# Optimization experiments

Hardware: AMD Instinct MI355X
Metric: run time of the kernel (lower is better)

The kernel has to match this reference:

```python
import jax, jax.numpy as jnp
import numpy as np

# Dims from init_kwargs / input_specs
C_IN, H, W = 128, 224, 224
C_OUT, KH, KW = 256, 3, 3
STRIDE = 1  # padding='valid'


def setup_inputs() -> dict:
    key = jax.random.key(0)
    k1, k2 = jax.random.split(key)
    x = jax.random.normal(k1, (C_IN, H, W), dtype=jnp.float32)
    kernels = jax.random.normal(k2, (C_OUT, C_IN, KH, KW), dtype=jnp.float32) * 0.05
    return {"x": x, "kernels": kernels}


def reference(x, kernels):
    # Original does im2col + matmul, which is exactly a valid cross-correlation
    # (no kernel flip). Express it as a direct conv: (1,C,H,W) * (O,I,kh,kw).
    out = jax.lax.conv_general_dilated(
        x[None],                      # (1, C_in, H, W)
        kernels,                      # (C_out, C_in, KH, KW)
        window_strides=(STRIDE, STRIDE),
        padding="VALID",
        dimension_numbers=("NCHW", "OIHW", "NCHW"),
    )
    return out[0]                     # (C_out, H_out, W_out) = (256, 222, 222)
```

## Files before the change

kernel.cpp:

```cpp
#include <hip/hip_runtime.h>

#define CIN   128
#define HH    224
#define WW    224
#define COUT  256
#define HO    222
#define WO    222
#define HWSZ  (224 * 224)
#define PLANE (224 * 224 * 64)

typedef unsigned short u16;
typedef unsigned int   u32;
typedef __bf16  bf16x8 __attribute__((ext_vector_type(8)));
typedef float   f32x4  __attribute__((ext_vector_type(4)));

__device__ __forceinline__ u16 f2bf(float f) {
  union { float f; u32 u; } v; v.f = f;
  u32 u = v.u;
  return (u16)((u + 0x7FFFu + ((u >> 16) & 1u)) >> 16);
}

__global__ void prep(const float* __restrict__ x, const float* __restrict__ w,
                     u16* __restrict__ xp, u16* __restrict__ wp) {
  const int t = threadIdx.x;
  if (blockIdx.x < 448) {
    const int h  = blockIdx.x >> 1;
    const int ch = blockIdx.x & 1;
    __shared__ u16 tileT[224][72];
#pragma unroll
    for (int i = 0; i < 14; ++i) {
      int idx = i * 256 + t;
      int c   = idx / 56;
      int wq  = idx % 56;
      float4 v = *(const float4*)(&x[(size_t)(ch * 64 + c) * HWSZ + h * WW + wq * 4]);
      tileT[wq * 4 + 0][c] = f2bf(v.x);
      tileT[wq * 4 + 1][c] = f2bf(v.y);
      tileT[wq * 4 + 2][c] = f2bf(v.z);
      tileT[wq * 4 + 3][c] = f2bf(v.w);
    }
    __syncthreads();
#pragma unroll
    for (int i = 0; i < 7; ++i) {
      int idx  = i * 256 + t;
      int ww   = idx >> 3;
      int jcp  = idx & 7;
      int jsrc = (jcp ^ (ww & 7)) * 8;
      uint4 v = *(const uint4*)(&tileT[ww][jsrc]);
      *(uint4*)(&xp[(size_t)ch * PLANE + (size_t)(h * WW + ww) * 64 + jcp * 8]) = v;
    }
  } else {
    int u    = (blockIdx.x - 448) * 256 + t;
    int jcp  = u & 7;
    int mr   = (u >> 3) & 127;
    int rest = u >> 10;
    int kw   = rest % 3;
    int q    = rest / 3;
    int ch   = q & 1;
    int r    = q >> 1;
    int kh   = r % 3;
    int mt   = r / 3;
    int oc   = mt * 128 + mr;
    int cb   = ch * 64 + (jcp ^ (mr & 7)) * 8;
    u16 o[8];
#pragma unroll
    for (int e = 0; e < 8; ++e)
      o[e] = f2bf(w[((size_t)(oc * CIN + cb + e) * 3 + kh) * 3 + kw]);
    uint4 v;
    v.x = (u32)o[0] | ((u32)o[1] << 16);
    v.y = (u32)o[2] | ((u32)o[3] << 16);
    v.z = (u32)o[4] | ((u32)o[5] << 16);
    v.w = (u32)o[6] | ((u32)o[7] << 16);
    *(uint4*)(&wp[(size_t)u * 8]) = v;
  }
}

__device__ __forceinline__ void lds_dma16(const u16* g, u16* l) {
  __builtin_amdgcn_global_load_lds(
      reinterpret_cast<__attribute__((address_space(1))) u32*>(
          reinterpret_cast<uintptr_t>(g)),
      reinterpret_cast<__attribute__((address_space(3))) u32*>(
          reinterpret_cast<uintptr_t>(l)),
      16, 0, 0);
}

__global__ __launch_bounds__(256, 4) void conv_mfma(const u16* __restrict__ wp,
                                                    const u16* __restrict__ xp,
                                                    float* __restrict__ out) {
  __shared__ u16 ldsB[2][8192];

  const int tid  = threadIdx.x;
  const int lane = tid & 63;
  const int wave = tid >> 6;
  const int quad = lane >> 4;
  const int lr   = lane & 15;

  const int bx  = blockIdx.x;
  const int xcd = bx & 7;
  const int u   = xcd * 111 + (bx >> 3);
  const int oh  = u >> 2;
  const int mt  = (u >> 1) & 1;
  const int nt  = u & 1;

  f32x4 acc[2][7];
#pragma unroll
  for (int i = 0; i < 2; ++i)
#pragma unroll
    for (int j = 0; j < 7; ++j) acc[i][j] = {0.f, 0.f, 0.f, 0.f};

  int swA[2];
#pragma unroll
  for (int ks = 0; ks < 2; ++ks)
    swA[ks] = ((ks * 4 + quad) ^ (lr & 7)) << 3;

  {
    const u16* g0 = xp + (size_t)oh * (WW * 64) + nt * (112 * 64);
#pragma unroll
    for (int uu = 0; uu < 4; ++uu) {
      const int unit = wave * 4 + uu;
      lds_dma16(g0 + unit * 512 + lane * 8, &ldsB[0][unit * 512]);
    }
  }
  __syncthreads();

#pragma unroll 1
  for (int s = 0; s < 6; ++s) {
    const int cur = s & 1;

    if (s < 5) {
      const int sn  = s + 1;
      const u16* gn = xp + (size_t)(sn & 1) * PLANE +
                      (size_t)(oh + (sn >> 1)) * (WW * 64) + nt * (112 * 64);
      u16* dst = &ldsB[cur ^ 1][0];
#pragma unroll
      for (int uu = 0; uu < 4; ++uu) {
        const int unit = wave * 4 + uu;
        lds_dma16(gn + unit * 512 + lane * 8, dst + unit * 512);
      }
    }

    const int ch = s & 1;
    const int kh = s >> 1;

    const u16* Ab = wp + (size_t)((mt * 3 + kh) * 2 + ch) * 24576 +
                    wave * 2048 + lr * 64;
    const u16* Bb = &ldsB[cur][0];

#pragma unroll
    for (int kw = 0; kw < 3; ++kw) {
      const int bq  = (lr + kw) * 64;
      const int sw7 = (lr + kw) & 7;
#pragma unroll
      for (int ks = 0; ks < 2; ++ks) {
        const int swB = ((ks * 4 + quad) ^ sw7) << 3;
        bf16x8 af[2], bg[7];
#pragma unroll
        for (int i = 0; i < 2; ++i)
          af[i] = *reinterpret_cast<const bf16x8*>(Ab + kw * 8192 + i * 1024 + swA[ks]);
#pragma unroll
        for (int j = 0; j < 7; ++j)
          bg[j] = *reinterpret_cast<const bf16x8*>(Bb + bq + j * 1024 + swB);
#pragma unroll
        for (int i = 0; i < 2; ++i)
#pragma unroll
          for (int j = 0; j < 7; ++j)
            acc[i][j] = __builtin_amdgcn_mfma_f32_16x16x32_bf16(af[i], bg[j], acc[i][j], 0, 0, 0);
      }
    }

    __syncthreads();
  }

  const int mb = mt * 128 + wave * 32;
#pragma unroll
  for (int i = 0; i < 2; ++i) {
#pragma unroll
    for (int j = 0; j < 7; ++j) {
      const int col = nt * 112 + j * 16 + lr;
      if (col < WO) {
        float* op = out + (size_t)(mb + i * 16 + quad * 4) * (HO * WO) +
                    (size_t)oh * WO + col;
#pragma unroll
        for (int r = 0; r < 4; ++r)
          op[(size_t)r * (HO * WO)] = acc[i][j][r];
      }
    }
  }
}

__global__ void conv_naive(const float* __restrict__ x, const float* __restrict__ w,
                           float* __restrict__ out) {
  int idx = blockIdx.x * 256 + threadIdx.x;
  if (idx >= COUT * HO * WO) return;
  int ow  = idx % WO;
  int tmp = idx / WO;
  int oh  = tmp % HO;
  int oc  = tmp / HO;
  float s = 0.f;
  for (int c = 0; c < CIN; ++c)
    for (int kh = 0; kh < 3; ++kh) {
      const float* xr = &x[(size_t)(c * HH + oh + kh) * WW + ow];
      const float* wr = &w[((size_t)(oc * CIN + c) * 3 + kh) * 3];
      s += xr[0] * wr[0] + xr[1] * wr[1] + xr[2] * wr[2];
    }
  out[idx] = s;
}

extern "C" void kernel_launch(void* const* d_in, const int* in_sizes, int n_in,
                              void* d_out, int out_size, void* d_ws, size_t ws_size,
                              hipStream_t stream) {
  const float* x    = (const float*)d_in[0];
  const float* kern = (const float*)d_in[1];
  float* out        = (float*)d_out;

  const size_t WP_BYTES = (size_t)36864 * 16;
  const size_t XP_BYTES = (size_t)2 * PLANE * 2;

  if (ws_size >= WP_BYTES + XP_BYTES) {
    u16* wp = (u16*)d_ws;
    u16* xp = (u16*)((char*)d_ws + WP_BYTES);
    hipLaunchKernelGGL(prep, dim3(592), dim3(256), 0, stream, x, kern, xp, wp);
    hipLaunchKernelGGL(conv_mfma, dim3(888), dim3(256), 0, stream, wp, xp, out);
  } else {
    int total = COUT * HO * WO;
    hipLaunchKernelGGL(conv_naive, dim3((total + 255) / 256), dim3(256), 0, stream,
                       x, kern, out);
  }
}
```

Before: 112.5 us.

## Replicate packed weights per XCD and map prep rows to consuming XCDs

The prep kernel now writes eight copies of the packed bf16 weights, one per XCD, and the conv kernel reads the copy for its own XCD. This is meant to keep weight reads in the local L2 instead of crossing XCDs. The input-transpose blocks are also reordered so each XCD writes the rows its conv blocks will later read, which should leave those rows in the same L2. In exchange the weight prep does eight times the conversion work and workspace grows, and the L2 locality depends on blocks being dispatched to XCDs round-robin.

```diff
diff --git a/kernel.cpp b/kernel.cpp
--- a/kernel.cpp
+++ b/kernel.cpp
@@ -8,6 +8,7 @@
 #define WO    222
 #define HWSZ  (224 * 224)
 #define PLANE (224 * 224 * 64)
+#define WPC   294912
 
 typedef unsigned short u16;
 typedef unsigned int   u32;
@@ -23,9 +24,18 @@
 __global__ void prep(const float* __restrict__ x, const float* __restrict__ w,
                      u16* __restrict__ xp, u16* __restrict__ wp) {
   const int t = threadIdx.x;
-  if (blockIdx.x < 448) {
-    const int h  = blockIdx.x >> 1;
-    const int ch = blockIdx.x & 1;
+  if (blockIdx.x < 452) {
+    int ch, h;
+    if (blockIdx.x < 448) {
+      const int xcd = blockIdx.x & 7;
+      const int idx = blockIdx.x >> 3;
+      ch = idx & 1;
+      h  = ((111 * xcd) >> 2) + (idx >> 1);
+    } else {
+      const int i2 = blockIdx.x - 448;
+      ch = i2 & 1;
+      h  = 222 + (i2 >> 1);
+    }
     __shared__ u16 tileT[224][72];
 #pragma unroll
     for (int i = 0; i < 14; ++i) {
@@ -49,28 +59,35 @@
       *(uint4*)(&xp[(size_t)ch * PLANE + (size_t)(h * WW + ww) * 64 + jcp * 8]) = v;
     }
   } else {
-    int u    = (blockIdx.x - 448) * 256 + t;
-    int jcp  = u & 7;
-    int mr   = (u >> 3) & 127;
-    int rest = u >> 10;
-    int kw   = rest % 3;
-    int q    = rest / 3;
-    int ch   = q & 1;
-    int r    = q >> 1;
-    int kh   = r % 3;
-    int mt   = r / 3;
-    int oc   = mt * 128 + mr;
-    int cb   = ch * 64 + (jcp ^ (mr & 7)) * 8;
-    u16 o[8];
-#pragma unroll
-    for (int e = 0; e < 8; ++e)
-      o[e] = f2bf(w[((size_t)(oc * CIN + cb + e) * 3 + kh) * 3 + kw]);
-    uint4 v;
-    v.x = (u32)o[0] | ((u32)o[1] << 16);
-    v.y = (u32)o[2] | ((u32)o[3] << 16);
-    v.z = (u32)o[4] | ((u32)o[5] << 16);
-    v.w = (u32)o[6] | ((u32)o[7] << 16);
-    *(uint4*)(&wp[(size_t)u * 8]) = v;
+    const int wb = blockIdx.x - 452;
+    const int c  = blockIdx.x & 7;
+    const int r  = wb >> 3;
+    u16* wpx = wp + (size_t)c * WPC;
+#pragma unroll
+    for (int e = 0; e < 8; ++e) {
+      int u    = r * 2048 + t * 8 + e;
+      int jcp  = u & 7;
+      int mr   = (u >> 3) & 127;
+      int rest = u >> 10;
+      int kw   = rest % 3;
+      int q    = rest / 3;
+      int ch   = q & 1;
+      int rr   = q >> 1;
+      int kh   = rr % 3;
+      int mt   = rr / 3;
+      int oc   = mt * 128 + mr;
+      int cb   = ch * 64 + (jcp ^ (mr & 7)) * 8;
+      u16 o[8];
+#pragma unroll
+      for (int k = 0; k < 8; ++k)
+        o[k] = f2bf(w[((size_t)(oc * CIN + cb + k) * 3 + kh) * 3 + kw]);
+      uint4 v;
+      v.x = (u32)o[0] | ((u32)o[1] << 16);
+      v.y = (u32)o[2] | ((u32)o[3] << 16);
+      v.z = (u32)o[4] | ((u32)o[5] << 16);
+      v.w = (u32)o[6] | ((u32)o[7] << 16);
+      *(uint4*)(&wpx[(size_t)u * 8]) = v;
+    }
   }
 }
 
@@ -101,6 +118,8 @@
   const int mt  = (u >> 1) & 1;
   const int nt  = u & 1;
 
+  const u16* wpx = wp + (size_t)xcd * WPC;
+
   f32x4 acc[2][7];
 #pragma unroll
   for (int i = 0; i < 2; ++i)
@@ -141,7 +160,7 @@
     const int ch = s & 1;
     const int kh = s >> 1;
 
-    const u16* Ab = wp + (size_t)((mt * 3 + kh) * 2 + ch) * 24576 +
+    const u16* Ab = wpx + (size_t)((mt * 3 + kh) * 2 + ch) * 24576 +
                     wave * 2048 + lr * 64;
     const u16* Bb = &ldsB[cur][0];
 
@@ -212,13 +231,13 @@
   const float* kern = (const float*)d_in[1];
   float* out        = (float*)d_out;
 
-  const size_t WP_BYTES = (size_t)36864 * 16;
+  const size_t WP_BYTES = (size_t)36864 * 16 * 8;
   const size_t XP_BYTES = (size_t)2 * PLANE * 2;
 
   if (ws_size >= WP_BYTES + XP_BYTES) {
     u16* wp = (u16*)d_ws;
     u16* xp = (u16*)((char*)d_ws + WP_BYTES);
-    hipLaunchKernelGGL(prep, dim3(592), dim3(256), 0, stream, x, kern, xp, wp);
+    hipLaunchKernelGGL(prep, dim3(596), dim3(256), 0, stream, x, kern, xp, wp);
     hipLaunchKernelGGL(conv_mfma, dim3(888), dim3(256), 0, stream, wp, xp, out);
   } else {
     int total = COUT * HO * WO;
```

Measured after the change: 120.5 us. 1.07x slower.

## Triple-buffer LDS input and prefetch weight fragments one stage ahead

Applied to the files above, without the earlier changes.

Replaces the double-buffered loop with a fully unrolled six-stage schedule. It uses three LDS buffers for the input rows and two register sets of weight fragments that are loaded one stage ahead. Explicit vmcnt waits, raw barriers and sched_barrier fences take the place of __syncthreads, so global loads for the next stage overlap the MFMA work of the current one. The extra weight-fragment registers force launch bounds down from 4 to 2 blocks per CU, which trades occupancy for latency hiding.

```diff
diff --git a/kernel.cpp b/kernel.cpp
--- a/kernel.cpp
+++ b/kernel.cpp
@@ -83,10 +83,14 @@
       16, 0, 0);
 }
 
-__global__ __launch_bounds__(256, 4) void conv_mfma(const u16* __restrict__ wp,
+#define VMCNT(n)  asm volatile("s_waitcnt vmcnt(" #n ")" ::: "memory")
+#define SCHED0    __builtin_amdgcn_sched_barrier(0)
+#define RAWBAR    __builtin_amdgcn_s_barrier()
+
+__global__ __launch_bounds__(256, 2) void conv_mfma(const u16* __restrict__ wp,
                                                     const u16* __restrict__ xp,
                                                     float* __restrict__ out) {
-  __shared__ u16 ldsB[2][8192];
+  __shared__ u16 ldsB[3][8192];
 
   const int tid  = threadIdx.x;
   const int lane = tid & 63;
@@ -112,63 +116,81 @@
   for (int ks = 0; ks < 2; ++ks)
     swA[ks] = ((ks * 4 + quad) ^ (lr & 7)) << 3;
 
-  {
-    const u16* g0 = xp + (size_t)oh * (WW * 64) + nt * (112 * 64);
-#pragma unroll
-    for (int uu = 0; uu < 4; ++uu) {
-      const int unit = wave * 4 + uu;
-      lds_dma16(g0 + unit * 512 + lane * 8, &ldsB[0][unit * 512]);
-    }
-  }
-  __syncthreads();
-
-#pragma unroll 1
-  for (int s = 0; s < 6; ++s) {
-    const int cur = s & 1;
-
-    if (s < 5) {
-      const int sn  = s + 1;
-      const u16* gn = xp + (size_t)(sn & 1) * PLANE +
-                      (size_t)(oh + (sn >> 1)) * (WW * 64) + nt * (112 * 64);
-      u16* dst = &ldsB[cur ^ 1][0];
-#pragma unroll
-      for (int uu = 0; uu < 4; ++uu) {
-        const int unit = wave * 4 + uu;
-        lds_dma16(gn + unit * 512 + lane * 8, dst + unit * 512);
-      }
-    }
-
-    const int ch = s & 1;
-    const int kh = s >> 1;
-
-    const u16* Ab = wp + (size_t)((mt * 3 + kh) * 2 + ch) * 24576 +
-                    wave * 2048 + lr * 64;
-    const u16* Bb = &ldsB[cur][0];
-
-#pragma unroll
-    for (int kw = 0; kw < 3; ++kw) {
-      const int bq  = (lr + kw) * 64;
-      const int sw7 = (lr + kw) & 7;
-#pragma unroll
-      for (int ks = 0; ks < 2; ++ks) {
-        const int swB = ((ks * 4 + quad) ^ sw7) << 3;
-        bf16x8 af[2], bg[7];
-#pragma unroll
-        for (int i = 0; i < 2; ++i)
-          af[i] = *reinterpret_cast<const bf16x8*>(Ab + kw * 8192 + i * 1024 + swA[ks]);
-#pragma unroll
-        for (int j = 0; j < 7; ++j)
-          bg[j] = *reinterpret_cast<const bf16x8*>(Bb + bq + j * 1024 + swB);
-#pragma unroll
-        for (int i = 0; i < 2; ++i)
-#pragma unroll
-          for (int j = 0; j < 7; ++j)
-            acc[i][j] = __builtin_amdgcn_mfma_f32_16x16x32_bf16(af[i], bg[j], acc[i][j], 0, 0, 0);
-      }
-    }
-
-    __syncthreads();
-  }
+  bf16x8 afA[3][2][2], afB[3][2][2];
+
+#define LOAD_AF(AF, sn) do {                                                   \
+    const u16* Ab_ = wp + (size_t)((mt * 3 + ((sn) >> 1)) * 2 + ((sn) & 1)) *  \
+                     24576 + wave * 2048 + lr * 64;                            \
+    _Pragma("unroll") for (int kw = 0; kw < 3; ++kw)                           \
+    _Pragma("unroll") for (int ks = 0; ks < 2; ++ks)                           \
+    _Pragma("unroll") for (int i = 0; i < 2; ++i)                              \
+      AF[kw][ks][i] = *reinterpret_cast<const bf16x8*>(                        \
+          Ab_ + kw * 8192 + i * 1024 + swA[ks]);                               \
+  } while (0)
+
+#define STAGE(sn) do {                                                         \
+    const u16* g_ = xp + (size_t)((sn) & 1) * PLANE +                          \
+                    (size_t)(oh + ((sn) >> 1)) * (WW * 64) + nt * (112 * 64);  \
+    u16* d_ = &ldsB[(sn) % 3][0];                                              \
+    _Pragma("unroll") for (int uu = 0; uu < 4; ++uu) {                         \
+      const int unit_ = wave * 4 + uu;                                         \
+      lds_dma16(g_ + unit_ * 512 + lane * 8, d_ + unit_ * 512);                \
+    }                                                                          \
+  } while (0)
+
+#define COMPUTE(s, AF) do {                                                    \
+    const u16* Bb_ = &ldsB[(s) % 3][0];                                        \
+    _Pragma("unroll") for (int kw = 0; kw < 3; ++kw) {                         \
+      const int bq_  = (lr + kw) * 64;                                         \
+      const int sw7_ = (lr + kw) & 7;                                          \
+      _Pragma("unroll") for (int ks = 0; ks < 2; ++ks) {                       \
+        const int swB_ = ((ks * 4 + quad) ^ sw7_) << 3;                        \
+        bf16x8 bg[7];                                                          \
+        _Pragma("unroll") for (int j = 0; j < 7; ++j)                          \
+          bg[j] = *reinterpret_cast<const bf16x8*>(Bb_ + bq_ + j * 1024 + swB_);\
+        _Pragma("unroll") for (int i = 0; i < 2; ++i)                          \
+        _Pragma("unroll") for (int j = 0; j < 7; ++j)                          \
+          acc[i][j] = __builtin_amdgcn_mfma_f32_16x16x32_bf16(                 \
+              AF[kw][ks][i], bg[j], acc[i][j], 0, 0, 0);                       \
+      }                                                                        \
+    }                                                                          \
+  } while (0)
+
+  STAGE(0);          SCHED0;
+  LOAD_AF(afA, 0);   SCHED0;
+  STAGE(1);          SCHED0;
+  VMCNT(4);          SCHED0;
+  RAWBAR;            SCHED0;
+
+  LOAD_AF(afB, 1);   SCHED0;
+  STAGE(2);          SCHED0;
+  COMPUTE(0, afA);
+  VMCNT(4);          SCHED0;
+  RAWBAR;            SCHED0;
+  LOAD_AF(afA, 2);   SCHED0;
+  STAGE(3);          SCHED0;
+  COMPUTE(1, afB);
+  VMCNT(4);          SCHED0;
+  RAWBAR;            SCHED0;
+  LOAD_AF(afB, 3);   SCHED0;
+  STAGE(4);          SCHED0;
+  COMPUTE(2, afA);
+  VMCNT(4);          SCHED0;
+  RAWBAR;            SCHED0;
+  LOAD_AF(afA, 4);   SCHED0;
+  STAGE(5);          SCHED0;
+  COMPUTE(3, afB);
+  VMCNT(4);          SCHED0;
+  RAWBAR;            SCHED0;
+  LOAD_AF(afB, 5);   SCHED0;
+  COMPUTE(4, afA);
+  VMCNT(0);          SCHED0;
+  RAWBAR;            SCHED0;
+  COMPUTE(5, afB);
+
+#undef LOAD_AF
+#undef STAGE
+#undef COMPUTE
 
   const int mb = mt * 128 + wave * 32;
 #pragma unroll
```

Result: slower. 116.4 us (+3.5%).

## Switch conv to 32x32x16 MFMA with 2x2 wave tiling and 128-wide N tiles

Applied to the files above, without the earlier changes.

Replaces the 16x16x32 MFMA tiling (each wave 32 rows by 112 cols) with 32x32x16 MFMA over a 2x2 wave grid, each wave covering 64 rows by 64 cols, and widens each block's N tile from 112 to 128 columns. The input LDS buffer grows to 10240 elements per stage, loaded in 5 DMA units per wave. Occupancy hint drops to 3 blocks per SM. The goal is fewer A/B fragment loads per MFMA and better MFMA efficiency, at the cost of redundant columns past 222 and a required workspace slack, since the last tile reads past the row end.

```diff
diff --git a/kernel.cpp b/kernel.cpp
--- a/kernel.cpp
+++ b/kernel.cpp
@@ -12,7 +12,7 @@
 typedef unsigned short u16;
 typedef unsigned int   u32;
 typedef __bf16  bf16x8 __attribute__((ext_vector_type(8)));
-typedef float   f32x4  __attribute__((ext_vector_type(4)));
+typedef float   f32x16 __attribute__((ext_vector_type(16)));
 
 __device__ __forceinline__ u16 f2bf(float f) {
   union { float f; u32 u; } v; v.f = f;
@@ -83,16 +83,18 @@
       16, 0, 0);
 }
 
-__global__ __launch_bounds__(256, 4) void conv_mfma(const u16* __restrict__ wp,
+__global__ __launch_bounds__(256, 3) void conv_mfma(const u16* __restrict__ wp,
                                                     const u16* __restrict__ xp,
                                                     float* __restrict__ out) {
-  __shared__ u16 ldsB[2][8192];
+  __shared__ u16 ldsB[2][10240];
 
   const int tid  = threadIdx.x;
   const int lane = tid & 63;
   const int wave = tid >> 6;
-  const int quad = lane >> 4;
-  const int lr   = lane & 15;
+  const int l31  = lane & 31;
+  const int hl   = lane >> 5;
+  const int wm   = wave >> 1;
+  const int wn   = wave & 1;
 
   const int bx  = blockIdx.x;
   const int xcd = bx & 7;
@@ -101,22 +103,28 @@
   const int mt  = (u >> 1) & 1;
   const int nt  = u & 1;
 
-  f32x4 acc[2][7];
+  f32x16 acc[2][2];
 #pragma unroll
   for (int i = 0; i < 2; ++i)
 #pragma unroll
-    for (int j = 0; j < 7; ++j) acc[i][j] = {0.f, 0.f, 0.f, 0.f};
-
-  int swA[2];
-#pragma unroll
-  for (int ks = 0; ks < 2; ++ks)
-    swA[ks] = ((ks * 4 + quad) ^ (lr & 7)) << 3;
+    for (int j = 0; j < 2; ++j)
+#pragma unroll
+      for (int r = 0; r < 16; ++r) acc[i][j][r] = 0.f;
+
+  int swA[4];
+#pragma unroll
+  for (int ks = 0; ks < 4; ++ks)
+    swA[ks] = ((ks * 2 + hl) ^ (lane & 7)) << 3;
+  int rowA[2];
+#pragma unroll
+  for (int i = 0; i < 2; ++i)
+    rowA[i] = (wm * 64 + i * 32 + l31) * 64;
 
   {
-    const u16* g0 = xp + (size_t)oh * (WW * 64) + nt * (112 * 64);
-#pragma unroll
-    for (int uu = 0; uu < 4; ++uu) {
-      const int unit = wave * 4 + uu;
+    const u16* g0 = xp + (size_t)oh * (WW * 64) + nt * (128 * 64);
+#pragma unroll
+    for (int uu = 0; uu < 5; ++uu) {
+      const int unit = wave * 5 + uu;
       lds_dma16(g0 + unit * 512 + lane * 8, &ldsB[0][unit * 512]);
     }
   }
@@ -129,11 +137,11 @@
     if (s < 5) {
       const int sn  = s + 1;
       const u16* gn = xp + (size_t)(sn & 1) * PLANE +
-                      (size_t)(oh + (sn >> 1)) * (WW * 64) + nt * (112 * 64);
+                      (size_t)(oh + (sn >> 1)) * (WW * 64) + nt * (128 * 64);
       u16* dst = &ldsB[cur ^ 1][0];
 #pragma unroll
-      for (int uu = 0; uu < 4; ++uu) {
-        const int unit = wave * 4 + uu;
+      for (int uu = 0; uu < 5; ++uu) {
+        const int unit = wave * 5 + uu;
         lds_dma16(gn + unit * 512 + lane * 8, dst + unit * 512);
       }
     }
@@ -141,47 +149,48 @@
     const int ch = s & 1;
     const int kh = s >> 1;
 
-    const u16* Ab = wp + (size_t)((mt * 3 + kh) * 2 + ch) * 24576 +
-                    wave * 2048 + lr * 64;
+    const u16* Ab = wp + (size_t)((mt * 3 + kh) * 2 + ch) * 24576;
     const u16* Bb = &ldsB[cur][0];
 
 #pragma unroll
     for (int kw = 0; kw < 3; ++kw) {
-      const int bq  = (lr + kw) * 64;
-      const int sw7 = (lr + kw) & 7;
-#pragma unroll
-      for (int ks = 0; ks < 2; ++ks) {
-        const int swB = ((ks * 4 + quad) ^ sw7) << 3;
-        bf16x8 af[2], bg[7];
+      const int scol = (l31 + kw) & 7;
+      const int cbas = (wn * 64 + l31 + kw) * 64;
+#pragma unroll
+      for (int ks = 0; ks < 4; ++ks) {
+        const int swB = ((ks * 2 + hl) ^ scol) << 3;
+        bf16x8 af[2], bg[2];
 #pragma unroll
         for (int i = 0; i < 2; ++i)
-          af[i] = *reinterpret_cast<const bf16x8*>(Ab + kw * 8192 + i * 1024 + swA[ks]);
-#pragma unroll
-        for (int j = 0; j < 7; ++j)
-          bg[j] = *reinterpret_cast<const bf16x8*>(Bb + bq + j * 1024 + swB);
+          af[i] = *reinterpret_cast<const bf16x8*>(Ab + kw * 8192 + rowA[i] + swA[ks]);
+#pragma unroll
+        for (int j = 0; j < 2; ++j)
+          bg[j] = *reinterpret_cast<const bf16x8*>(Bb + cbas + j * 2048 + swB);
 #pragma unroll
         for (int i = 0; i < 2; ++i)
 #pragma unroll
-          for (int j = 0; j < 7; ++j)
-            acc[i][j] = __builtin_amdgcn_mfma_f32_16x16x32_bf16(af[i], bg[j], acc[i][j], 0, 0, 0);
+          for (int j = 0; j < 2; ++j)
+            acc[i][j] = __builtin_amdgcn_mfma_f32_32x32x16_bf16(af[i], bg[j],
+                                                                acc[i][j], 0, 0, 0);
       }
     }
 
     __syncthreads();
   }
 
-  const int mb = mt * 128 + wave * 32;
+  const int mb = mt * 128 + wm * 64;
 #pragma unroll
   for (int i = 0; i < 2; ++i) {
 #pragma unroll
-    for (int j = 0; j < 7; ++j) {
-      const int col = nt * 112 + j * 16 + lr;
+    for (int j = 0; j < 2; ++j) {
+      const int col = nt * 128 + wn * 64 + j * 32 + l31;
       if (col < WO) {
-        float* op = out + (size_t)(mb + i * 16 + quad * 4) * (HO * WO) +
-                    (size_t)oh * WO + col;
-#pragma unroll
-        for (int r = 0; r < 4; ++r)
-          op[(size_t)r * (HO * WO)] = acc[i][j][r];
+        float* op = out + (size_t)oh * WO + col;
+#pragma unroll
+        for (int r = 0; r < 16; ++r) {
+          const int row = mb + i * 32 + (r & 3) + 8 * (r >> 2) + 4 * hl;
+          op[(size_t)row * (HO * WO)] = acc[i][j][r];
+        }
       }
     }
   }
@@ -214,8 +223,9 @@
 
   const size_t WP_BYTES = (size_t)36864 * 16;
   const size_t XP_BYTES = (size_t)2 * PLANE * 2;
-
-  if (ws_size >= WP_BYTES + XP_BYTES) {
+  const size_t SLACK    = 65536;
+
+  if (ws_size >= WP_BYTES + XP_BYTES + SLACK) {
     u16* wp = (u16*)d_ws;
     u16* xp = (u16*)((char*)d_ws + WP_BYTES);
     hipLaunchKernelGGL(prep, dim3(592), dim3(256), 0, stream, x, kern, xp, wp);
```

Result: slower. 135.1 us (+20.1%).
